# Optimization experiments

Hardware: AMD Instinct MI355X
Metric: run time of the kernel (lower is better)

## Reference

```python
import jax, jax.numpy as jnp
import numpy as np

B, Q, K = 4, 128, 1024
DQ, DK, DV, H = 512, 512, 512, 256
NEG_INF = -1e6


def setup_inputs() -> dict:
    key = jax.random.key(0)
    ks = jax.random.split(key, 6)
    queries = jax.random.normal(ks[0], (B, Q, DQ), dtype=jnp.float32)
    keys = jax.random.normal(ks[1], (B, K, DK), dtype=jnp.float32)
    values = jax.random.normal(ks[2], (B, K, DV), dtype=jnp.float32)
    valid_lens = jax.random.randint(ks[3], (B,), 1, K + 1, dtype=jnp.int32)
    # Learned params (Dense use_bias=False): W_q [DQ,H], W_k [DK,H], w_v [H] (Dense(1) squeezed)
    Wq = jax.random.normal(ks[4], (DQ, H), dtype=jnp.float32) / np.sqrt(DQ)
    Wk = jax.random.normal(ks[5], (DK, H), dtype=jnp.float32) / np.sqrt(DK)
    wv = jax.random.normal(jax.random.fold_in(key, 7), (H,), dtype=jnp.float32) / np.sqrt(H)
    return {"queries": queries, "keys": keys, "values": values,
            "valid_lens": valid_lens, "Wq": Wq, "Wk": Wk, "wv": wv}


def reference(queries, keys, values, valid_lens, Wq, Wk, wv):
    q = queries @ Wq                       # [B,Q,H]
    k = keys @ Wk                          # [B,K,H]
    feats = jnp.tanh(q[:, :, None, :] + k[:, None, :, :])   # [B,Q,K,H]
    scores = jnp.einsum('bqkh,h->bqk', feats, wv)            # [B,Q,K]
    mask = jnp.arange(scores.shape[-1]) < valid_lens[:, None, None]  # [B,1,K]
    scores = jnp.where(mask, scores, NEG_INF)
    attn = jax.nn.softmax(scores, axis=-1)                   # [B,Q,K]
    # dropout is identity at inference
    return attn @ values                                     # [B,Q,DV]
```

## Files before the change

kernel.cpp:

```cpp
#include <hip/hip_runtime.h>

#define Bn 4
#define Qn 128
#define Kn 1024
#define Dn 512
#define Hn 256

__device__ __forceinline__ float fast_tanh(float x) {
    float e = __expf(2.0f * x);
    return 1.0f - 2.0f * __builtin_amdgcn_rcpf(1.0f + e);
}

#define PBK 64

__global__ __launch_bounds__(512, 4) void proj_kernel(
    const float* __restrict__ queries, const float* __restrict__ keys,
    const float* __restrict__ Wq, const float* __restrict__ Wk,
    const int* __restrict__ valid_lens,
    float* __restrict__ qproj, float* __restrict__ kproj)
{
    const int blk = blockIdx.x;
    const int nt = blk & 3;
    const int mt = blk >> 2;
    const int t = threadIdx.x;
    const float* Asrc; const float* W; float* Dst;
    int m0;
    if (mt < 8) {
        m0 = mt * 64;
        Asrc = queries; W = Wq; Dst = qproj;
    } else {
        int r0 = (mt - 8) * 64;
        int b = r0 >> 10;
        if ((r0 & 1023) >= valid_lens[b]) return;
        m0 = r0;
        Asrc = keys; W = Wk; Dst = kproj;
    }
    const int n0 = nt * 64;

    __shared__ float s_a[PBK][68];
    __shared__ float s_b[PBK][64];

    const int tt   = t & 255;
    const int kh   = t >> 8;
    const int trow = tt >> 4;
    const int tcol = tt & 15;
    const int kklo = kh << 5;

    const int lrow = t >> 4;
    const int lc4  = t & 15;

    float acc[4][4] = {{0.f}};
    float4 ra[2], rb[2];

    #pragma unroll
    for (int i = 0; i < 2; ++i) {
        ra[i] = *(const float4*)(Asrc + (size_t)(m0 + lrow + i * 32) * Dn + lc4 * 4);
        rb[i] = *(const float4*)(W + (size_t)(lrow + i * 32) * Hn + n0 + lc4 * 4);
    }

    for (int kt = 0; kt < 8; ++kt) {
        __syncthreads();
        #pragma unroll
        for (int i = 0; i < 2; ++i) {
            int row = lrow + i * 32;
            s_a[lc4 * 4 + 0][row] = ra[i].x;
            s_a[lc4 * 4 + 1][row] = ra[i].y;
            s_a[lc4 * 4 + 2][row] = ra[i].z;
            s_a[lc4 * 4 + 3][row] = ra[i].w;
            *(float4*)&s_b[row][lc4 * 4] = rb[i];
        }
        __syncthreads();
        if (kt < 7) {
            const int d0n = (kt + 1) * PBK;
            #pragma unroll
            for (int i = 0; i < 2; ++i) {
                ra[i] = *(const float4*)(Asrc + (size_t)(m0 + lrow + i * 32) * Dn + d0n + lc4 * 4);
                rb[i] = *(const float4*)(W + (size_t)(d0n + lrow + i * 32) * Hn + n0 + lc4 * 4);
            }
        }
        #pragma unroll
        for (int kk = 0; kk < 32; ++kk) {
            float4 a4 = *(const float4*)&s_a[kklo + kk][trow * 4];
            float4 b4 = *(const float4*)&s_b[kklo + kk][tcol * 4];
            float a[4] = {a4.x, a4.y, a4.z, a4.w};
            float b[4] = {b4.x, b4.y, b4.z, b4.w};
            #pragma unroll
            for (int i = 0; i < 4; ++i)
                #pragma unroll
                for (int j = 0; j < 4; ++j)
                    acc[i][j] += a[i] * b[j];
        }
    }

    __syncthreads();
    float* red = &s_a[0][0];
    if (kh) {
        #pragma unroll
        for (int i = 0; i < 4; ++i)
            #pragma unroll
            for (int j = 0; j < 4; ++j)
                red[tt * 17 + i * 4 + j] = acc[i][j];
    }
    __syncthreads();
    if (!kh) {
        #pragma unroll
        for (int i = 0; i < 4; ++i) {
            float4 o;
            o.x = acc[i][0] + red[tt * 17 + i * 4 + 0];
            o.y = acc[i][1] + red[tt * 17 + i * 4 + 1];
            o.z = acc[i][2] + red[tt * 17 + i * 4 + 2];
            o.w = acc[i][3] + red[tt * 17 + i * 4 + 3];
            *(float4*)(Dst + (size_t)(m0 + trow * 4 + i) * Hn + n0 + tcol * 4) = o;
        }
    }
}

#define SK_KT 16
#define SK_PAD 260

__global__ __launch_bounds__(256) void score_kernel(
    const float* __restrict__ qproj, const float* __restrict__ kproj,
    const float* __restrict__ wv, const int* __restrict__ valid_lens,
    float* __restrict__ escores, float* __restrict__ rowsum)
{
    const int blk = blockIdx.x;
    const int kt = blk & 63;
    const int qt = (blk >> 6) & 31;
    const int b  = blk >> 11;
    const int vlen = valid_lens[b];
    const int k0 = kt * SK_KT;
    if (k0 >= vlen) return;
    const int q0 = qt * 4;
    const int t = threadIdx.x;

    __shared__ float s_k[SK_KT * SK_PAD];
    __shared__ float s_q[4 * Hn];
    __shared__ float s_wv[Hn];

    {
        const float4* src = reinterpret_cast<const float4*>(
            kproj + ((size_t)b * Kn + k0) * Hn);
        #pragma unroll
        for (int i = 0; i < 4; ++i) {
            int idx = t + i * 256;
            int row = idx >> 6, c4 = idx & 63;
            *reinterpret_cast<float4*>(&s_k[row * SK_PAD + c4 * 4]) = src[idx];
        }
        reinterpret_cast<float4*>(s_q)[t] = reinterpret_cast<const float4*>(
            qproj + ((size_t)b * Qn + q0) * Hn)[t];
        if (t < 64)
            reinterpret_cast<float4*>(s_wv)[t] =
                reinterpret_cast<const float4*>(wv)[t];
    }
    __syncthreads();

    const int wave = t >> 6;
    const int lane = t & 63;
    const int kloc = lane & 15;
    const int hq   = lane >> 4;

    const float4* kr = reinterpret_cast<const float4*>(&s_k[kloc * SK_PAD + hq * 64]);
    const float4* qr = reinterpret_cast<const float4*>(&s_q[wave * Hn + hq * 64]);
    const float4* wr = reinterpret_cast<const float4*>(&s_wv[hq * 64]);

    float s = 0.0f;
    #pragma unroll
    for (int i = 0; i < 16; ++i) {
        float4 kv = kr[i];
        float4 qv = qr[i];
        float4 wq = wr[i];
        s += wq.x * fast_tanh(qv.x + kv.x);
        s += wq.y * fast_tanh(qv.y + kv.y);
        s += wq.z * fast_tanh(qv.z + kv.z);
        s += wq.w * fast_tanh(qv.w + kv.w);
    }
    s += __shfl_xor(s, 16, 64);
    s += __shfl_xor(s, 32, 64);

    const int k = k0 + kloc;
    float e = 0.0f;
    if (lane < 16 && k < vlen) {
        e = __expf(s);
        escores[((size_t)b * Qn + q0 + wave) * Kn + k] = e;
    }
    #pragma unroll
    for (int off = 32; off; off >>= 1)
        e += __shfl_xor(e, off, 64);
    if (lane == 0)
        atomicAdd(&rowsum[b * Qn + q0 + wave], e);
}

__global__ __launch_bounds__(256) void av_part_kernel(
    const float* __restrict__ escores, const float* __restrict__ values,
    float* __restrict__ parts)
{
    const int blk = blockIdx.x;
    const int kc = blk & 3;
    const int dh = (blk >> 2) & 1;
    const int qt = (blk >> 3) & 15;
    const int b  = blk >> 7;
    const int t = threadIdx.x;
    const int q0 = qt * 8;
    const int kb = kc * 256;
    const int d  = dh * 256 + t;

    __shared__ float s_e[8][256];
    #pragma unroll
    for (int i = 0; i < 2; ++i) {
        int idx = t + i * 256;
        int row = idx >> 6, c4 = idx & 63;
        *(float4*)&s_e[row][c4 * 4] = *(const float4*)(
            escores + ((size_t)(b * Qn + q0 + row)) * Kn + kb + c4 * 4);
    }
    __syncthreads();

    const float* vb = values + ((size_t)b * Kn + kb) * Dn + d;
    float acc[8] = {0.f};
    #pragma unroll 2
    for (int k = 0; k < 256; k += 4) {
        float v0 = vb[(size_t)(k + 0) * Dn];
        float v1 = vb[(size_t)(k + 1) * Dn];
        float v2 = vb[(size_t)(k + 2) * Dn];
        float v3 = vb[(size_t)(k + 3) * Dn];
        #pragma unroll
        for (int j = 0; j < 8; ++j) {
            float4 e4 = *(const float4*)&s_e[j][k];
            acc[j] += e4.x * v0 + e4.y * v1 + e4.z * v2 + e4.w * v3;
        }
    }
    float* pp = parts + (size_t)kc * (Bn * Qn * Dn)
                      + ((size_t)(b * Qn + q0)) * Dn + d;
    #pragma unroll
    for (int j = 0; j < 8; ++j)
        pp[(size_t)j * Dn] = acc[j];
}

__global__ __launch_bounds__(256) void reduce_kernel(
    const float* __restrict__ parts, const float* __restrict__ rowsum,
    float* __restrict__ out)
{
    const int idx = blockIdx.x * 256 + threadIdx.x;
    const int row = (idx * 4) >> 9;
    const float inv = __builtin_amdgcn_rcpf(rowsum[row]);
    const float4* p = (const float4*)parts;
    float4 a = p[idx];
    float4 b = p[idx + 65536];
    float4 c = p[idx + 131072];
    float4 d = p[idx + 196608];
    float4 o;
    o.x = (a.x + b.x + c.x + d.x) * inv;
    o.y = (a.y + b.y + c.y + d.y) * inv;
    o.z = (a.z + b.z + c.z + d.z) * inv;
    o.w = (a.w + b.w + c.w + d.w) * inv;
    ((float4*)out)[idx] = o;
}

extern "C" void kernel_launch(void* const* d_in, const int* in_sizes, int n_in,
                              void* d_out, int out_size, void* d_ws, size_t ws_size,
                              hipStream_t stream) {
    const float* queries    = (const float*)d_in[0];
    const float* keys       = (const float*)d_in[1];
    const float* values     = (const float*)d_in[2];
    const int*   valid_lens = (const int*)  d_in[3];
    const float* Wq         = (const float*)d_in[4];
    const float* Wk         = (const float*)d_in[5];
    const float* wv         = (const float*)d_in[6];
    float* out = (float*)d_out;

    float* qproj   = (float*)d_ws;
    float* kproj   = qproj + Bn * Qn * Hn;
    float* escores = kproj + Bn * Kn * Hn;
    float* rowsum  = escores + Bn * Qn * Kn;
    float* parts   = kproj;

    hipMemsetAsync(escores, 0, (size_t)(Bn * Qn * Kn + Bn * Qn) * sizeof(float),
                   stream);
    proj_kernel<<<288, 512, 0, stream>>>(queries, keys, Wq, Wk, valid_lens,
                                         qproj, kproj);
    score_kernel<<<Bn * 32 * 64, 256, 0, stream>>>(qproj, kproj, wv,
                                                   valid_lens, escores, rowsum);
    av_part_kernel<<<512, 256, 0, stream>>>(escores, values, parts);
    reduce_kernel<<<256, 256, 0, stream>>>(parts, rowsum, out);
}
```

Before: 157.1 us.

## Split projection GEMM over K and fuse AV reduction via atomics

Result: faster. 153.4 us (-2.3%).

```diff
diff --git a/kernel.cpp b/kernel.cpp
--- a/kernel.cpp
+++ b/kernel.cpp
@@ -17,25 +17,30 @@
     const float* __restrict__ queries, const float* __restrict__ keys,
     const float* __restrict__ Wq, const float* __restrict__ Wk,
     const int* __restrict__ valid_lens,
-    float* __restrict__ qproj, float* __restrict__ kproj)
+    float* __restrict__ proj0, float* __restrict__ proj1)
 {
     const int blk = blockIdx.x;
-    const int nt = blk & 3;
-    const int mt = blk >> 2;
+    const int kc = blk & 1;
+    const int nt = (blk >> 1) & 3;
+    const int mt = blk >> 3;
     const int t = threadIdx.x;
-    const float* Asrc; const float* W; float* Dst;
-    int m0;
+    const float* Asrc; const float* W;
+    int m0, drow;
     if (mt < 8) {
         m0 = mt * 64;
-        Asrc = queries; W = Wq; Dst = qproj;
+        drow = m0;
+        Asrc = queries; W = Wq;
     } else {
         int r0 = (mt - 8) * 64;
         int b = r0 >> 10;
         if ((r0 & 1023) >= valid_lens[b]) return;
         m0 = r0;
-        Asrc = keys; W = Wk; Dst = kproj;
+        drow = 512 + r0;
+        Asrc = keys; W = Wk;
     }
     const int n0 = nt * 64;
+    const int k0 = kc * 256;
+    float* Dst = (kc ? proj1 : proj0) + (size_t)drow * Hn;
 
     __shared__ float s_a[PBK][68];
     __shared__ float s_b[PBK][64];
@@ -54,11 +59,11 @@
 
     #pragma unroll
     for (int i = 0; i < 2; ++i) {
-        ra[i] = *(const float4*)(Asrc + (size_t)(m0 + lrow + i * 32) * Dn + lc4 * 4);
-        rb[i] = *(const float4*)(W + (size_t)(lrow + i * 32) * Hn + n0 + lc4 * 4);
-    }
-
-    for (int kt = 0; kt < 8; ++kt) {
+        ra[i] = *(const float4*)(Asrc + (size_t)(m0 + lrow + i * 32) * Dn + k0 + lc4 * 4);
+        rb[i] = *(const float4*)(W + (size_t)(k0 + lrow + i * 32) * Hn + n0 + lc4 * 4);
+    }
+
+    for (int kt = 0; kt < 4; ++kt) {
         __syncthreads();
         #pragma unroll
         for (int i = 0; i < 2; ++i) {
@@ -70,8 +75,8 @@
             *(float4*)&s_b[row][lc4 * 4] = rb[i];
         }
         __syncthreads();
-        if (kt < 7) {
-            const int d0n = (kt + 1) * PBK;
+        if (kt < 3) {
+            const int d0n = k0 + (kt + 1) * PBK;
             #pragma unroll
             for (int i = 0; i < 2; ++i) {
                 ra[i] = *(const float4*)(Asrc + (size_t)(m0 + lrow + i * 32) * Dn + d0n + lc4 * 4);
@@ -110,7 +115,7 @@
             o.y = acc[i][1] + red[tt * 17 + i * 4 + 1];
             o.z = acc[i][2] + red[tt * 17 + i * 4 + 2];
             o.w = acc[i][3] + red[tt * 17 + i * 4 + 3];
-            *(float4*)(Dst + (size_t)(m0 + trow * 4 + i) * Hn + n0 + tcol * 4) = o;
+            *(float4*)(Dst + (size_t)(trow * 4 + i) * Hn + n0 + tcol * 4) = o;
         }
     }
 }
@@ -119,7 +124,7 @@
 #define SK_PAD 260
 
 __global__ __launch_bounds__(256) void score_kernel(
-    const float* __restrict__ qproj, const float* __restrict__ kproj,
+    const float* __restrict__ proj0, const float* __restrict__ proj1,
     const float* __restrict__ wv, const int* __restrict__ valid_lens,
     float* __restrict__ escores, float* __restrict__ rowsum)
 {
@@ -138,16 +143,25 @@
     __shared__ float s_wv[Hn];
 
     {
-        const float4* src = reinterpret_cast<const float4*>(
-            kproj + ((size_t)b * Kn + k0) * Hn);
+        const float4* k0p = reinterpret_cast<const float4*>(
+            proj0 + ((size_t)512 + (size_t)b * Kn + k0) * Hn);
+        const float4* k1p = reinterpret_cast<const float4*>(
+            proj1 + ((size_t)512 + (size_t)b * Kn + k0) * Hn);
         #pragma unroll
         for (int i = 0; i < 4; ++i) {
             int idx = t + i * 256;
             int row = idx >> 6, c4 = idx & 63;
-            *reinterpret_cast<float4*>(&s_k[row * SK_PAD + c4 * 4]) = src[idx];
-        }
-        reinterpret_cast<float4*>(s_q)[t] = reinterpret_cast<const float4*>(
-            qproj + ((size_t)b * Qn + q0) * Hn)[t];
+            float4 a = k0p[idx];
+            float4 c = k1p[idx];
+            a.x += c.x; a.y += c.y; a.z += c.z; a.w += c.w;
+            *reinterpret_cast<float4*>(&s_k[row * SK_PAD + c4 * 4]) = a;
+        }
+        float4 qa = reinterpret_cast<const float4*>(
+            proj0 + ((size_t)b * Qn + q0) * Hn)[t];
+        float4 qb = reinterpret_cast<const float4*>(
+            proj1 + ((size_t)b * Qn + q0) * Hn)[t];
+        qa.x += qb.x; qa.y += qb.y; qa.z += qb.z; qa.w += qb.w;
+        reinterpret_cast<float4*>(s_q)[t] = qa;
         if (t < 64)
             reinterpret_cast<float4*>(s_wv)[t] =
                 reinterpret_cast<const float4*>(wv)[t];
@@ -190,9 +204,9 @@
         atomicAdd(&rowsum[b * Qn + q0 + wave], e);
 }
 
-__global__ __launch_bounds__(256) void av_part_kernel(
+__global__ __launch_bounds__(256) void av_kernel(
     const float* __restrict__ escores, const float* __restrict__ values,
-    float* __restrict__ parts)
+    const float* __restrict__ rowsum, float* __restrict__ out)
 {
     const int blk = blockIdx.x;
     const int kc = blk & 3;
@@ -228,31 +242,12 @@
             acc[j] += e4.x * v0 + e4.y * v1 + e4.z * v2 + e4.w * v3;
         }
     }
-    float* pp = parts + (size_t)kc * (Bn * Qn * Dn)
-                      + ((size_t)(b * Qn + q0)) * Dn + d;
-    #pragma unroll
-    for (int j = 0; j < 8; ++j)
-        pp[(size_t)j * Dn] = acc[j];
-}
-
-__global__ __launch_bounds__(256) void reduce_kernel(
-    const float* __restrict__ parts, const float* __restrict__ rowsum,
-    float* __restrict__ out)
-{
-    const int idx = blockIdx.x * 256 + threadIdx.x;
-    const int row = (idx * 4) >> 9;
-    const float inv = __builtin_amdgcn_rcpf(rowsum[row]);
-    const float4* p = (const float4*)parts;
-    float4 a = p[idx];
-    float4 b = p[idx + 65536];
-    float4 c = p[idx + 131072];
-    float4 d = p[idx + 196608];
-    float4 o;
-    o.x = (a.x + b.x + c.x + d.x) * inv;
-    o.y = (a.y + b.y + c.y + d.y) * inv;
-    o.z = (a.z + b.z + c.z + d.z) * inv;
-    o.w = (a.w + b.w + c.w + d.w) * inv;
-    ((float4*)out)[idx] = o;
+    float* op = out + ((size_t)(b * Qn + q0)) * Dn + d;
+    #pragma unroll
+    for (int j = 0; j < 8; ++j) {
+        float inv = __builtin_amdgcn_rcpf(rowsum[b * Qn + q0 + j]);
+        atomicAdd(op + (size_t)j * Dn, acc[j] * inv);
+    }
 }
 
 extern "C" void kernel_launch(void* const* d_in, const int* in_sizes, int n_in,
@@ -267,18 +262,18 @@
     const float* wv         = (const float*)d_in[6];
     float* out = (float*)d_out;
 
-    float* qproj   = (float*)d_ws;
-    float* kproj   = qproj + Bn * Qn * Hn;
-    float* escores = kproj + Bn * Kn * Hn;
-    float* rowsum  = escores + Bn * Qn * Kn;
-    float* parts   = kproj;
+    const size_t PROJ_F = (size_t)4608 * Hn;
+    float* proj0   = (float*)d_ws;
+    float* proj1   = proj0 + PROJ_F;
+    float* escores = proj1 + PROJ_F;
+    float* rowsum  = escores + (size_t)Bn * Qn * Kn;
 
     hipMemsetAsync(escores, 0, (size_t)(Bn * Qn * Kn + Bn * Qn) * sizeof(float),
                    stream);
-    proj_kernel<<<288, 512, 0, stream>>>(queries, keys, Wq, Wk, valid_lens,
-                                         qproj, kproj);
-    score_kernel<<<Bn * 32 * 64, 256, 0, stream>>>(qproj, kproj, wv,
+    hipMemsetAsync(out, 0, (size_t)Bn * Qn * Dn * sizeof(float), stream);
+    proj_kernel<<<576, 512, 0, stream>>>(queries, keys, Wq, Wk, valid_lens,
+                                         proj0, proj1);
+    score_kernel<<<Bn * 32 * 64, 256, 0, stream>>>(proj0, proj1, wv,
                                                    valid_lens, escores, rowsum);
-    av_part_kernel<<<512, 256, 0, stream>>>(escores, values, parts);
-    reduce_kernel<<<256, 256, 0, stream>>>(parts, rowsum, out);
-}
+    av_kernel<<<512, 256, 0, stream>>>(escores, values, rowsum, out);
+}
```
